# Kernel tuning notes

Measured on AMD Instinct MI355X. Metric: run time of the kernel, lower is better.

The kernel has to match this reference:

```python
import jax, jax.numpy as jnp
import numpy as np

H_DIM = 256
NUM_HEADS = 8
HEAD_DIM = H_DIM // NUM_HEADS
BN_EPS = 1e-5
SCALE = float(np.sqrt(HEAD_DIM))


def _lens():
    # 512 graphs, ragged vertex counts cycling 32/64/96/128 -> 40960 total rows
    return np.tile(np.array([32, 64, 96, 128], dtype=np.int64), 128)


def _pad(x, lens):
    # gather ragged rows of x [total, D] into padded [B, Lmax, D]; mask [B, Lmax]
    B = lens.shape[0]
    L = int(lens.max())
    off = np.zeros(B, np.int64)
    off[1:] = np.cumsum(lens)[:-1]
    pos = np.arange(L)
    idx = off[:, None] + np.minimum(pos[None, :], lens[:, None] - 1)
    mask = pos[None, :] < lens[:, None]
    return x[jnp.asarray(idx)], jnp.asarray(mask)


def _flat_idx(lens):
    # (graph_id, position) for every real row, to un-pad back to ragged layout
    b = np.repeat(np.arange(lens.shape[0]), lens)
    i = np.concatenate([np.arange(int(l)) for l in lens])
    return jnp.asarray(b), jnp.asarray(i)


def _forward(src_h, dst_h, src_lens, dst_lens,
             W1, b1, gamma1, beta1, W2, b2, gamma2, beta2):
    src_pad, src_mask = _pad(src_h, src_lens)   # [B, Ls, H]
    dst_pad, _ = _pad(dst_h, dst_lens)          # [B, Ld, H]
    B, Ls, _ = src_pad.shape
    Ld = dst_pad.shape[1]
    # NOTE: original torch code zips self.proj but never applies it, so
    # q = raw dst, k = v = raw src.  The .view(1, head_dim, heads, N) on the
    # channel-major tensor splits feature f as f = d*NUM_HEADS + h.
    q = dst_pad.reshape(B, Ld, HEAD_DIM, NUM_HEADS)
    k = src_pad.reshape(B, Ls, HEAD_DIM, NUM_HEADS)
    v = k
    scores = jnp.einsum('bndh,bmdh->bhnm', q, k) / SCALE
    scores = jnp.where(src_mask[:, None, None, :], scores, jnp.float32(-1e30))
    attn = jax.nn.softmax(scores, axis=-1)
    out = jnp.einsum('bhnm,bmdh->bndh', attn, v).reshape(B, Ld, H_DIM)
    bidx, iidx = _flat_idx(dst_lens)
    h_msg = out[bidx, iidx]                     # [total_dst, H] ragged again
    h = dst_h
    z = jnp.concatenate([h, h_msg], axis=-1)    # [N, 2H]
    y = z @ W1.T + b1
    y = gamma1 * (y - y.mean(0)) * jax.lax.rsqrt(y.var(0) + BN_EPS) + beta1
    y = jax.nn.relu(y)
    y = y @ W2.T + b2
    y = gamma2 * (y - y.mean(0)) * jax.lax.rsqrt(y.var(0) + BN_EPS) + beta2
    return h + y


def setup_inputs() -> dict:
    lens = _lens()
    N = int(lens.sum())
    ks = jax.random.split(jax.random.key(0), 4)
    return {
        'src_h': jax.random.normal(ks[0], (N, H_DIM), jnp.float32),
        'dst_h': jax.random.normal(ks[1], (N, H_DIM), jnp.float32),
        'src_num_verts': jnp.asarray(lens, jnp.int32),
        'dst_num_verts': jnp.asarray(lens, jnp.int32),
        'W1': jax.random.normal(ks[2], (H_DIM, 2 * H_DIM), jnp.float32) / np.float32(np.sqrt(2 * H_DIM)),
        'b1': jnp.zeros((H_DIM,), jnp.float32),
        'gamma1': jnp.ones((H_DIM,), jnp.float32),
        'beta1': jnp.zeros((H_DIM,), jnp.float32),
        'W2': jax.random.normal(ks[3], (H_DIM, H_DIM), jnp.float32) / np.float32(np.sqrt(H_DIM)),
        'b2': jnp.zeros((H_DIM,), jnp.float32),
        'gamma2': jnp.ones((H_DIM,), jnp.float32),
        'beta2': jnp.zeros((H_DIM,), jnp.float32),
    }


def reference(src_h, dst_h, src_num_verts, dst_num_verts,
              W1, b1, gamma1, beta1, W2, b2, gamma2, beta2):
    # segment lengths are static metadata (torch.split takes a Python list)
    src_lens = np.asarray(jax.device_get(src_num_verts), np.int64)
    dst_lens = np.asarray(jax.device_get(dst_num_verts), np.int64)
    return _forward(src_h, dst_h, src_lens, dst_lens,
                    W1, b1, gamma1, beta1, W2, b2, gamma2, beta2)
```

## Files before the change

### kernel.cpp

```cpp
#include <hip/hip_runtime.h>
#include <cstddef>

#define H 256
#define NHEADS 8
#define HD 32

typedef __attribute__((ext_vector_type(8))) short bf16x8;
typedef __attribute__((ext_vector_type(4))) float f32x4;

__device__ __forceinline__ float bf2f(unsigned short s) {
    unsigned u = ((unsigned)s) << 16; return __builtin_bit_cast(float, u);
}
__device__ __forceinline__ float bfe2f(short s) {
    unsigned u = ((unsigned)(unsigned short)s) << 16; return __builtin_bit_cast(float, u);
}
__device__ __forceinline__ unsigned short f2bf(float x) {
    unsigned u = __builtin_bit_cast(unsigned, x);
    u += 0x7fffu + ((u >> 16) & 1u);
    return (unsigned short)(u >> 16);
}
__device__ __forceinline__ void gl_lds16(const void* g, void* l) {
    __builtin_amdgcn_global_load_lds(
        (const __attribute__((address_space(1))) void*)g,
        (__attribute__((address_space(3))) void*)l, 16, 0, 0);
}

__global__ __launch_bounds__(512) void scan_zero_kernel(
    const int* __restrict__ slen, const int* __restrict__ dlen,
    int* __restrict__ soff, int* __restrict__ doff,
    float* __restrict__ stats, int B)
{
    __shared__ int ss[512], dd[512];
    const int t = threadIdx.x;
    const int sv = (t < B) ? slen[t] : 0;
    const int dv = (t < B) ? dlen[t] : 0;
    ss[t] = sv; dd[t] = dv;
    __syncthreads();
    for (int o = 1; o < 512; o <<= 1) {
        int a = (t >= o) ? ss[t - o] : 0;
        int b = (t >= o) ? dd[t - o] : 0;
        __syncthreads();
        ss[t] += a; dd[t] += b;
        __syncthreads();
    }
    if (t < B) { soff[t] = ss[t] - sv; doff[t] = dd[t] - dv; }
    stats[t] = 0.f;
    stats[t + 512] = 0.f;
}

__global__ __launch_bounds__(256) void prepass_kernel(
    const float* __restrict__ src, const float* __restrict__ dst,
    unsigned short* __restrict__ KT, unsigned short* __restrict__ VT2,
    unsigned short* __restrict__ QT, int N)
{
    __shared__ unsigned short pl[8 * 64 * 40];
    const int t = threadIdx.x;
    const int rb = blockIdx.x * 64;
    const int isrc = (blockIdx.y == 0);
    const float* __restrict__ in = isrc ? src : dst;
    unsigned short* __restrict__ T = isrc ? KT : QT;
    #pragma unroll
    for (int i = 0; i < 16; ++i) {
        const int idx = t + i * 256;
        const int row = idx >> 6, f4 = idx & 63;
        const float4 v = ((const float4*)in)[(size_t)(rb + row) * 64 + f4];
        const int f0 = f4 * 4, h0 = f0 & 7, d = f0 >> 3;
        pl[(h0 + 0) * 2560 + row * 40 + d] = f2bf(v.x);
        pl[(h0 + 1) * 2560 + row * 40 + d] = f2bf(v.y);
        pl[(h0 + 2) * 2560 + row * 40 + d] = f2bf(v.z);
        pl[(h0 + 3) * 2560 + row * 40 + d] = f2bf(v.w);
    }
    __syncthreads();
    #pragma unroll
    for (int i = 0; i < 8; ++i) {
        const int idx = t + i * 256;
        const int h = idx >> 8, rem = idx & 255, row = rem >> 2, c = rem & 3;
        const bf16x8 val = *(const bf16x8*)&pl[h * 2560 + row * 40 + c * 8];
        *(bf16x8*)&T[(size_t)(h * N + rb + row) * 32 + c * 8] = val;
    }
    if (isrc) {
        #pragma unroll
        for (int i = 0; i < 8; ++i) {
            const int idx = t + i * 256;
            const int h = idx >> 8, rem = idx & 255, d = rem >> 3, nc = rem & 7;
            unsigned short tmp[8];
            #pragma unroll
            for (int j = 0; j < 8; ++j) tmp[j] = pl[h * 2560 + (nc * 8 + j) * 40 + d];
            ushort4 lo, hi;
            lo.x = tmp[0]; lo.y = tmp[1]; lo.z = tmp[2]; lo.w = tmp[3];
            hi.x = tmp[4]; hi.y = tmp[5]; hi.z = tmp[6]; hi.w = tmp[7];
            *(ushort4*)&VT2[(size_t)(h * 32 + d) * N + rb + nc * 8] = lo;
            *(ushort4*)&VT2[(size_t)(h * 32 + d) * N + rb + nc * 8 + 4] = hi;
        }
    }
}

__global__ __launch_bounds__(256) void cvtW_kernel(
    const float* __restrict__ W1, const float* __restrict__ W2,
    unsigned short* __restrict__ W1p, unsigned short* __restrict__ W2bf)
{
    const int idx = blockIdx.x * 256 + threadIdx.x;
    if (idx < 131072) {
        const int kp = idx & 511, c = idx >> 9;
        const int half = kp >> 8, r = kp & 255, hh = r >> 5, d = r & 31;
        W1p[(size_t)c * 512 + kp] = f2bf(W1[(size_t)c * 512 + half * 256 + d * 8 + hh]);
    } else {
        const int i2 = idx - 131072;
        W2bf[i2] = f2bf(W2[i2]);
    }
}

template<int LS>
__device__ __forceinline__ void attn_body(
    const unsigned short* __restrict__ KT, const unsigned short* __restrict__ QT,
    const unsigned short* __restrict__ VT2, unsigned short* __restrict__ OT,
    unsigned short* __restrict__ Ps, int N, int so, int df, int Ld, int h, int lane)
{
    constexpr int MT = LS / 16, CH = LS / 32;
    const int lr = lane & 15, lq = lane >> 4;
    const float iscale = 0.17677669529663687f;

    bf16x8 kf[MT];
    #pragma unroll
    for (int mt = 0; mt < MT; ++mt)
        kf[mt] = *(const bf16x8*)&KT[(size_t)(h * N + so + mt * 16 + lr) * 32 + lq * 8];
    bf16x8 vf[CH][2];
    #pragma unroll
    for (int c = 0; c < CH; ++c)
        #pragma unroll
        for (int dt = 0; dt < 2; ++dt)
            vf[c][dt] = *(const bf16x8*)&VT2[(size_t)(h * 32 + dt * 16 + lr) * N + so + c * 32 + lq * 8];

    const int NT = Ld >> 4;
    for (int nt = 0; nt < NT; ++nt) {
        const bf16x8 qf = *(const bf16x8*)&QT[(size_t)(h * N + df + nt * 16 + lr) * 32 + lq * 8];
        f32x4 s[MT];
        #pragma unroll
        for (int mt = 0; mt < MT; ++mt) {
            f32x4 z = {0.f, 0.f, 0.f, 0.f};
            s[mt] = __builtin_amdgcn_mfma_f32_16x16x32_bf16(kf[mt], qf, z, 0, 0, 0);
        }
        float mx = -INFINITY;
        #pragma unroll
        for (int mt = 0; mt < MT; ++mt)
            mx = fmaxf(mx, fmaxf(fmaxf(s[mt][0], s[mt][1]), fmaxf(s[mt][2], s[mt][3])));
        mx = fmaxf(mx, __shfl_xor(mx, 16));
        mx = fmaxf(mx, __shfl_xor(mx, 32));
        const float mxi = mx * iscale;
        float sum = 0.f;
        #pragma unroll
        for (int mt = 0; mt < MT; ++mt) {
            #pragma unroll
            for (int r = 0; r < 4; ++r) {
                const float e = __expf(s[mt][r] * iscale - mxi);
                s[mt][r] = e; sum += e;
            }
        }
        sum += __shfl_xor(sum, 16);
        sum += __shfl_xor(sum, 32);
        const float rinv = 1.f / sum;
        #pragma unroll
        for (int mt = 0; mt < MT; ++mt) {
            uint2 p;
            p.x = ((unsigned)f2bf(s[mt][0])) | (((unsigned)f2bf(s[mt][1])) << 16);
            p.y = ((unsigned)f2bf(s[mt][2])) | (((unsigned)f2bf(s[mt][3])) << 16);
            *(uint2*)&Ps[lr * 136 + mt * 16 + lq * 4] = p;
        }
        __asm__ volatile("" ::: "memory");
        __builtin_amdgcn_wave_barrier();
        f32x4 o0 = {0.f, 0.f, 0.f, 0.f}, o1 = {0.f, 0.f, 0.f, 0.f};
        #pragma unroll
        for (int c = 0; c < CH; ++c) {
            const bf16x8 pa = *(const bf16x8*)&Ps[lr * 136 + c * 32 + lq * 8];
            o0 = __builtin_amdgcn_mfma_f32_16x16x32_bf16(pa, vf[c][0], o0, 0, 0, 0);
            o1 = __builtin_amdgcn_mfma_f32_16x16x32_bf16(pa, vf[c][1], o1, 0, 0, 0);
        }
        __asm__ volatile("" ::: "memory");
        __builtin_amdgcn_wave_barrier();
        #pragma unroll
        for (int r = 0; r < 4; ++r) {
            const float rv = __shfl(rinv, lq * 4 + r);
            const int row = df + nt * 16 + lq * 4 + r;
            OT[(size_t)(h * N + row) * 32 + lr]      = f2bf(o0[r] * rv);
            OT[(size_t)(h * N + row) * 32 + 16 + lr] = f2bf(o1[r] * rv);
        }
    }
}

__global__ __launch_bounds__(256) void attn_mfma(
    const unsigned short* __restrict__ KT, const unsigned short* __restrict__ QT,
    const unsigned short* __restrict__ VT2, unsigned short* __restrict__ OT,
    const int* __restrict__ soff, const int* __restrict__ doff,
    const int* __restrict__ slen, const int* __restrict__ dlen, int N)
{
    __shared__ unsigned short Ps[4][16 * 136];
    const int b = blockIdx.x >> 1, half = blockIdx.x & 1;
    const int w = threadIdx.x >> 6, lane = threadIdx.x & 63;
    const int h = half * 4 + w;
    const int Ls = slen[b], Ld = dlen[b], so = soff[b], df = doff[b];
    switch (Ls) {
        case 32:  attn_body<32> (KT, QT, VT2, OT, Ps[w], N, so, df, Ld, h, lane); break;
        case 64:  attn_body<64> (KT, QT, VT2, OT, Ps[w], N, so, df, Ld, h, lane); break;
        case 96:  attn_body<96> (KT, QT, VT2, OT, Ps[w], N, so, df, Ld, h, lane); break;
        default:  attn_body<128>(KT, QT, VT2, OT, Ps[w], N, so, df, Ld, h, lane); break;
    }
}

__global__ __launch_bounds__(256) void gemm1_mfma(
    const unsigned short* __restrict__ QT, const unsigned short* __restrict__ OT,
    const unsigned short* __restrict__ W, const float* __restrict__ bias,
    unsigned short* __restrict__ out, float* __restrict__ sum, float* __restrict__ sq,
    int N)
{
    __shared__ unsigned short Abuf[8 * 512];
    __shared__ unsigned short Bbuf[8 * 512];
    const int tid = threadIdx.x;
    const int w = tid >> 6, lane = tid & 63;
    const int rowBase = blockIdx.y * 128, colBase = blockIdx.x * 128;
    const int lr = lane & 15, lq = lane >> 4;
    const int wm = w >> 1, wn = w & 1;

    f32x4 acc[4][4];
    #pragma unroll
    for (int i = 0; i < 4; ++i)
        #pragma unroll
        for (int j = 0; j < 4; ++j) { f32x4 z = {0.f, 0.f, 0.f, 0.f}; acc[i][j] = z; }

    #pragma unroll
    for (int phase = 0; phase < 2; ++phase) {
        const unsigned short* __restrict__ Ap = phase ? OT : QT;
        const int wOff = phase * 256;
        for (int kb = 0; kb < 256; kb += 32) {
            const int hh = (kb >> 5) + (lq >> 2);
            const int dd = (lq & 3) * 8;
            #pragma unroll
            for (int s = 0; s < 2; ++s) {
                const int sub = 2 * w + s;
                const unsigned short* ga = Ap + (size_t)(hh * N + rowBase + sub * 16 + lr) * 32 + dd;
                gl_lds16(ga, &Abuf[sub * 512]);
                const unsigned short* gb = W + (size_t)(colBase + sub * 16 + lr) * 512 + wOff + kb + lq * 8;
                gl_lds16(gb, &Bbuf[sub * 512]);
            }
            __syncthreads();
            bf16x8 af[4], bf[4];
            #pragma unroll
            for (int i = 0; i < 4; ++i) af[i] = *(const bf16x8*)&Abuf[(wm * 4 + i) * 512 + lane * 8];
            #pragma unroll
            for (int j = 0; j < 4; ++j) bf[j] = *(const bf16x8*)&Bbuf[(wn * 4 + j) * 512 + lane * 8];
            #pragma unroll
            for (int i = 0; i < 4; ++i)
                #pragma unroll
                for (int j = 0; j < 4; ++j)
                    acc[i][j] = __builtin_amdgcn_mfma_f32_16x16x32_bf16(af[i], bf[j], acc[i][j], 0, 0, 0);
            __syncthreads();
        }
    }
    const int col0 = colBase + wn * 64;
    #pragma unroll
    for (int j = 0; j < 4; ++j) {
        const int col = col0 + j * 16 + lr;
        const float bv = bias[col];
        float cs = 0.f, cq = 0.f;
        #pragma unroll
        for (int i = 0; i < 4; ++i) {
            const int row0 = rowBase + wm * 64 + i * 16 + lq * 4;
            #pragma unroll
            for (int r = 0; r < 4; ++r) {
                const float v = acc[i][j][r] + bv;
                cs += v; cq += v * v;
                out[(size_t)(row0 + r) * 256 + col] = f2bf(v);
            }
        }
        cs += __shfl_xor(cs, 16); cs += __shfl_xor(cs, 32);
        cq += __shfl_xor(cq, 16); cq += __shfl_xor(cq, 32);
        if (lq == 0) { atomicAdd(&sum[col], cs); atomicAdd(&sq[col], cq); }
    }
}

__global__ __launch_bounds__(256) void gemm2_mfma(
    const unsigned short* __restrict__ A2,
    const unsigned short* __restrict__ W, const float* __restrict__ bias,
    unsigned short* __restrict__ out, float* __restrict__ sum, float* __restrict__ sq)
{
    __shared__ unsigned short Abuf[8 * 512];
    __shared__ unsigned short Bbuf[8 * 512];
    const int tid = threadIdx.x;
    const int w = tid >> 6, lane = tid & 63;
    const int rowBase = blockIdx.y * 128, colBase = blockIdx.x * 128;
    const int lr = lane & 15, lq = lane >> 4;
    const int wm = w >> 1, wn = w & 1;

    f32x4 acc[4][4];
    #pragma unroll
    for (int i = 0; i < 4; ++i)
        #pragma unroll
        for (int j = 0; j < 4; ++j) { f32x4 z = {0.f, 0.f, 0.f, 0.f}; acc[i][j] = z; }

    for (int kb = 0; kb < 256; kb += 32) {
        #pragma unroll
        for (int s = 0; s < 2; ++s) {
            const int sub = 2 * w + s;
            const unsigned short* ga = A2 + (size_t)(rowBase + sub * 16 + lr) * 256 + kb + lq * 8;
            gl_lds16(ga, &Abuf[sub * 512]);
            const unsigned short* gb = W + (size_t)(colBase + sub * 16 + lr) * 256 + kb + lq * 8;
            gl_lds16(gb, &Bbuf[sub * 512]);
        }
        __syncthreads();
        bf16x8 af[4], bf[4];
        #pragma unroll
        for (int i = 0; i < 4; ++i) af[i] = *(const bf16x8*)&Abuf[(wm * 4 + i) * 512 + lane * 8];
        #pragma unroll
        for (int j = 0; j < 4; ++j) bf[j] = *(const bf16x8*)&Bbuf[(wn * 4 + j) * 512 + lane * 8];
        #pragma unroll
        for (int i = 0; i < 4; ++i)
            #pragma unroll
            for (int j = 0; j < 4; ++j)
                acc[i][j] = __builtin_amdgcn_mfma_f32_16x16x32_bf16(af[i], bf[j], acc[i][j], 0, 0, 0);
        __syncthreads();
    }
    const int col0 = colBase + wn * 64;
    #pragma unroll
    for (int j = 0; j < 4; ++j) {
        const int col = col0 + j * 16 + lr;
        const float bv = bias[col];
        float cs = 0.f, cq = 0.f;
        #pragma unroll
        for (int i = 0; i < 4; ++i) {
            const int row0 = rowBase + wm * 64 + i * 16 + lq * 4;
            #pragma unroll
            for (int r = 0; r < 4; ++r) {
                const float v = acc[i][j][r] + bv;
                cs += v; cq += v * v;
                out[(size_t)(row0 + r) * 256 + col] = f2bf(v);
            }
        }
        cs += __shfl_xor(cs, 16); cs += __shfl_xor(cs, 32);
        cq += __shfl_xor(cq, 16); cq += __shfl_xor(cq, 32);
        if (lq == 0) { atomicAdd(&sum[col], cs); atomicAdd(&sq[col], cq); }
    }
}

__global__ __launch_bounds__(256) void bnrelu_kernel(
    const unsigned short* __restrict__ y1,
    const float* __restrict__ sum, const float* __restrict__ sq,
    const float* __restrict__ gamma, const float* __restrict__ beta,
    unsigned short* __restrict__ out, int n8, float invN)
{
    const int i = blockIdx.x * 256 + threadIdx.x;
    if (i >= n8) return;
    const int j0 = (i & 31) * 8;
    const bf16x8 yv = ((const bf16x8*)y1)[i];
    short res[8];
    #pragma unroll
    for (int j = 0; j < 8; ++j) {
        const float mean = sum[j0 + j] * invN;
        const float var  = sq[j0 + j] * invN - mean * mean;
        const float rstd = rsqrtf(var + 1e-5f);
        const float sc = gamma[j0 + j] * rstd;
        const float sh = beta[j0 + j] - mean * sc;
        res[j] = (short)f2bf(fmaxf(bfe2f(yv[j]) * sc + sh, 0.f));
    }
    bf16x8 o;
    #pragma unroll
    for (int j = 0; j < 8; ++j) o[j] = res[j];
    ((bf16x8*)out)[i] = o;
}

__global__ __launch_bounds__(256) void epilogue_kernel(
    const float* __restrict__ dst, const unsigned short* __restrict__ y2,
    const float* __restrict__ sum, const float* __restrict__ sq,
    const float* __restrict__ gamma, const float* __restrict__ beta,
    float* __restrict__ out, int n8, float invN)
{
    const int i = blockIdx.x * 256 + threadIdx.x;
    if (i >= n8) return;
    const int j0 = (i & 31) * 8;
    const bf16x8 yv = ((const bf16x8*)y2)[i];
    const float4 d0 = ((const float4*)dst)[2 * i];
    const float4 d1 = ((const float4*)dst)[2 * i + 1];
    float o[8];
    const float dv[8] = {d0.x, d0.y, d0.z, d0.w, d1.x, d1.y, d1.z, d1.w};
    #pragma unroll
    for (int j = 0; j < 8; ++j) {
        const float mean = sum[j0 + j] * invN;
        const float var  = sq[j0 + j] * invN - mean * mean;
        const float rstd = rsqrtf(var + 1e-5f);
        const float sc = gamma[j0 + j] * rstd;
        const float sh = beta[j0 + j] - mean * sc;
        o[j] = dv[j] + bfe2f(yv[j]) * sc + sh;
    }
    float4 o0, o1;
    o0.x = o[0]; o0.y = o[1]; o0.z = o[2]; o0.w = o[3];
    o1.x = o[4]; o1.y = o[5]; o1.z = o[6]; o1.w = o[7];
    ((float4*)out)[2 * i]     = o0;
    ((float4*)out)[2 * i + 1] = o1;
}

extern "C" void kernel_launch(void* const* d_in, const int* in_sizes, int n_in,
                              void* d_out, int out_size, void* d_ws, size_t ws_size,
                              hipStream_t stream)
{
    const float* src_h  = (const float*)d_in[0];
    const float* dst_h  = (const float*)d_in[1];
    const int*   slen   = (const int*)d_in[2];
    const int*   dlen   = (const int*)d_in[3];
    const float* W1     = (const float*)d_in[4];
    const float* b1     = (const float*)d_in[5];
    const float* gamma1 = (const float*)d_in[6];
    const float* beta1  = (const float*)d_in[7];
    const float* W2     = (const float*)d_in[8];
    const float* b2     = (const float*)d_in[9];
    const float* gamma2 = (const float*)d_in[10];
    const float* beta2  = (const float*)d_in[11];
    float* out = (float*)d_out;

    const int N = in_sizes[1] / H;
    const int B = in_sizes[2];

    char* base = (char*)d_ws;
    int*   soff   = (int*)(base + 0);
    int*   doff   = (int*)(base + 2048);
    float* stats  = (float*)(base + 4096);
    unsigned short* W1p  = (unsigned short*)(base + 16384);
    unsigned short* W2bf = (unsigned short*)(base + 16384 + 262144);
    const size_t S = (size_t)N * H * sizeof(unsigned short);
    char* big = base + (1 << 20);
    unsigned short* KT  = (unsigned short*)(big);
    unsigned short* VT2 = (unsigned short*)(big + S);
    unsigned short* QT  = (unsigned short*)(big + 2 * S);
    unsigned short* OT  = (unsigned short*)(big + 3 * S);
    unsigned short* y1bf = KT;
    unsigned short* a2   = VT2;
    unsigned short* y2bf = QT;

    const float invN = 1.0f / (float)N;

    scan_zero_kernel<<<1, 512, 0, stream>>>(slen, dlen, soff, doff, stats, B);

    prepass_kernel<<<dim3(N / 64, 2), 256, 0, stream>>>(src_h, dst_h, KT, VT2, QT, N);
    cvtW_kernel<<<768, 256, 0, stream>>>(W1, W2, W1p, W2bf);

    attn_mfma<<<B * 2, 256, 0, stream>>>(KT, QT, VT2, OT, soff, doff, slen, dlen, N);

    dim3 ggrid(H / 128, N / 128);
    gemm1_mfma<<<ggrid, 256, 0, stream>>>(QT, OT, W1p, b1, y1bf, stats + 0, stats + 256, N);

    const int n8 = N * H / 8;
    bnrelu_kernel<<<(n8 + 255) / 256, 256, 0, stream>>>(
        y1bf, stats + 0, stats + 256, gamma1, beta1, a2, n8, invN);

    gemm2_mfma<<<ggrid, 256, 0, stream>>>(a2, W2bf, b2, y2bf, stats + 512, stats + 768);

    epilogue_kernel<<<(n8 + 255) / 256, 256, 0, stream>>>(
        dst_h, y2bf, stats + 512, stats + 768, gamma2, beta2, out, n8, invN);
}
```

Measured before the change: 286.6 us.

## Double-buffer LDS tiles in both MFMA GEMMs to overlap loads with compute

Both GEMM kernels now use two LDS buffers per operand. The next K-slice is issued with global_load_lds before computing on the current one, so memory latency can hide behind MFMA work. GEMM1's two-phase loop is flattened into a single 16-step K loop. This doubles LDS usage per block, which may lower occupancy, and the per-iteration barriers may still force load completion.

```diff
diff --git a/kernel.cpp b/kernel.cpp
--- a/kernel.cpp
+++ b/kernel.cpp
@@ -212,8 +212,8 @@
     unsigned short* __restrict__ out, float* __restrict__ sum, float* __restrict__ sq,
     int N)
 {
-    __shared__ unsigned short Abuf[8 * 512];
-    __shared__ unsigned short Bbuf[8 * 512];
+    __shared__ unsigned short Abuf[2][8 * 512];
+    __shared__ unsigned short Bbuf[2][8 * 512];
     const int tid = threadIdx.x;
     const int w = tid >> 6, lane = tid & 63;
     const int rowBase = blockIdx.y * 128, colBase = blockIdx.x * 128;
@@ -226,35 +226,42 @@
         #pragma unroll
         for (int j = 0; j < 4; ++j) { f32x4 z = {0.f, 0.f, 0.f, 0.f}; acc[i][j] = z; }
 
-    #pragma unroll
-    for (int phase = 0; phase < 2; ++phase) {
-        const unsigned short* __restrict__ Ap = phase ? OT : QT;
-        const int wOff = phase * 256;
-        for (int kb = 0; kb < 256; kb += 32) {
-            const int hh = (kb >> 5) + (lq >> 2);
-            const int dd = (lq & 3) * 8;
-            #pragma unroll
-            for (int s = 0; s < 2; ++s) {
-                const int sub = 2 * w + s;
-                const unsigned short* ga = Ap + (size_t)(hh * N + rowBase + sub * 16 + lr) * 32 + dd;
-                gl_lds16(ga, &Abuf[sub * 512]);
-                const unsigned short* gb = W + (size_t)(colBase + sub * 16 + lr) * 512 + wOff + kb + lq * 8;
-                gl_lds16(gb, &Bbuf[sub * 512]);
-            }
-            __syncthreads();
-            bf16x8 af[4], bf[4];
-            #pragma unroll
-            for (int i = 0; i < 4; ++i) af[i] = *(const bf16x8*)&Abuf[(wm * 4 + i) * 512 + lane * 8];
-            #pragma unroll
-            for (int j = 0; j < 4; ++j) bf[j] = *(const bf16x8*)&Bbuf[(wn * 4 + j) * 512 + lane * 8];
-            #pragma unroll
-            for (int i = 0; i < 4; ++i)
-                #pragma unroll
-                for (int j = 0; j < 4; ++j)
-                    acc[i][j] = __builtin_amdgcn_mfma_f32_16x16x32_bf16(af[i], bf[j], acc[i][j], 0, 0, 0);
-            __syncthreads();
-        }
-    }
+    auto stage = [&](int ks, int bi) {
+        const unsigned short* __restrict__ Ap = (ks < 8) ? QT : OT;
+        const int hh = ks & 7;
+        #pragma unroll
+        for (int s = 0; s < 2; ++s) {
+            const int sub = 2 * w + s;
+            gl_lds16(Ap + (size_t)(hh * N + rowBase + sub * 16 + lr) * 32 + lq * 8,
+                     &Abuf[bi][sub * 512]);
+            gl_lds16(W + (size_t)(colBase + sub * 16 + lr) * 512 + ks * 32 + lq * 8,
+                     &Bbuf[bi][sub * 512]);
+        }
+    };
+    auto compute = [&](int bi) {
+        bf16x8 af[4], bfr[4];
+        #pragma unroll
+        for (int i = 0; i < 4; ++i) af[i] = *(const bf16x8*)&Abuf[bi][(wm * 4 + i) * 512 + lane * 8];
+        #pragma unroll
+        for (int j = 0; j < 4; ++j) bfr[j] = *(const bf16x8*)&Bbuf[bi][(wn * 4 + j) * 512 + lane * 8];
+        #pragma unroll
+        for (int i = 0; i < 4; ++i)
+            #pragma unroll
+            for (int j = 0; j < 4; ++j)
+                acc[i][j] = __builtin_amdgcn_mfma_f32_16x16x32_bf16(af[i], bfr[j], acc[i][j], 0, 0, 0);
+    };
+
+    stage(0, 0);
+    __syncthreads();
+    for (int ks = 0; ks < 16; ks += 2) {
+        stage(ks + 1, 1);
+        compute(0);
+        __syncthreads();
+        if (ks + 2 < 16) stage(ks + 2, 0);
+        compute(1);
+        __syncthreads();
+    }
+
     const int col0 = colBase + wn * 64;
     #pragma unroll
     for (int j = 0; j < 4; ++j) {
@@ -282,8 +289,8 @@
     const unsigned short* __restrict__ W, const float* __restrict__ bias,
     unsigned short* __restrict__ out, float* __restrict__ sum, float* __restrict__ sq)
 {
-    __shared__ unsigned short Abuf[8 * 512];
-    __shared__ unsigned short Bbuf[8 * 512];
+    __shared__ unsigned short Abuf[2][8 * 512];
+    __shared__ unsigned short Bbuf[2][8 * 512];
     const int tid = threadIdx.x;
     const int w = tid >> 6, lane = tid & 63;
     const int rowBase = blockIdx.y * 128, colBase = blockIdx.x * 128;
@@ -296,28 +303,40 @@
         #pragma unroll
         for (int j = 0; j < 4; ++j) { f32x4 z = {0.f, 0.f, 0.f, 0.f}; acc[i][j] = z; }
 
-    for (int kb = 0; kb < 256; kb += 32) {
+    auto stage = [&](int ks, int bi) {
         #pragma unroll
         for (int s = 0; s < 2; ++s) {
             const int sub = 2 * w + s;
-            const unsigned short* ga = A2 + (size_t)(rowBase + sub * 16 + lr) * 256 + kb + lq * 8;
-            gl_lds16(ga, &Abuf[sub * 512]);
-            const unsigned short* gb = W + (size_t)(colBase + sub * 16 + lr) * 256 + kb + lq * 8;
-            gl_lds16(gb, &Bbuf[sub * 512]);
-        }
-        __syncthreads();
-        bf16x8 af[4], bf[4];
-        #pragma unroll
-        for (int i = 0; i < 4; ++i) af[i] = *(const bf16x8*)&Abuf[(wm * 4 + i) * 512 + lane * 8];
-        #pragma unroll
-        for (int j = 0; j < 4; ++j) bf[j] = *(const bf16x8*)&Bbuf[(wn * 4 + j) * 512 + lane * 8];
+            gl_lds16(A2 + (size_t)(rowBase + sub * 16 + lr) * 256 + ks * 32 + lq * 8,
+                     &Abuf[bi][sub * 512]);
+            gl_lds16(W + (size_t)(colBase + sub * 16 + lr) * 256 + ks * 32 + lq * 8,
+                     &Bbuf[bi][sub * 512]);
+        }
+    };
+    auto compute = [&](int bi) {
+        bf16x8 af[4], bfr[4];
+        #pragma unroll
+        for (int i = 0; i < 4; ++i) af[i] = *(const bf16x8*)&Abuf[bi][(wm * 4 + i) * 512 + lane * 8];
+        #pragma unroll
+        for (int j = 0; j < 4; ++j) bfr[j] = *(const bf16x8*)&Bbuf[bi][(wn * 4 + j) * 512 + lane * 8];
         #pragma unroll
         for (int i = 0; i < 4; ++i)
             #pragma unroll
             for (int j = 0; j < 4; ++j)
-                acc[i][j] = __builtin_amdgcn_mfma_f32_16x16x32_bf16(af[i], bf[j], acc[i][j], 0, 0, 0);
-        __syncthreads();
-    }
+                acc[i][j] = __builtin_amdgcn_mfma_f32_16x16x32_bf16(af[i], bfr[j], acc[i][j], 0, 0, 0);
+    };
+
+    stage(0, 0);
+    __syncthreads();
+    for (int ks = 0; ks < 8; ks += 2) {
+        stage(ks + 1, 1);
+        compute(0);
+        __syncthreads();
+        if (ks + 2 < 8) stage(ks + 2, 0);
+        compute(1);
+        __syncthreads();
+    }
+
     const int col0 = colBase + wn * 64;
     #pragma unroll
     for (int j = 0; j < 4; ++j) {
```

Result: no change. 281.2 us (-1.9%).
